# Optimization experiments

Measured on AMD Instinct MI355X. Metric: run time of the kernel, lower is better.

The kernel has to match this reference:

```python
import jax, jax.numpy as jnp
import numpy as np

B, T, C, H = 4, 2048, 1024, 16
D = C // H  # head dim = 64

def setup_inputs() -> dict:
    key = jax.random.key(0)
    k1, k2, k3 = jax.random.split(key, 3)
    s = 1.0 / np.sqrt(C)
    return {
        "x": jax.random.normal(k1, (B, T, C), dtype=jnp.float32),
        "W_attn": jax.random.normal(k2, (C, 3 * C), dtype=jnp.float32) * s,
        "b_attn": jnp.zeros((3 * C,), dtype=jnp.float32),
        "W_proj": jax.random.normal(k3, (C, C), dtype=jnp.float32) * s,
        "b_proj": jnp.zeros((C,), dtype=jnp.float32),
    }

def reference(x, W_attn, b_attn, W_proj, b_proj):
    qkv = x @ W_attn + b_attn                      # [B,T,3C]
    q, k, v = jnp.split(qkv, 3, axis=-1)
    # [B,T,C] -> [B,H,T,D]
    q = q.reshape(B, T, H, D).transpose(0, 2, 1, 3)
    k = k.reshape(B, T, H, D).transpose(0, 2, 1, 3)
    v = v.reshape(B, T, H, D).transpose(0, 2, 1, 3)
    scale = 1.0 / np.sqrt(D)
    att = jnp.einsum('bhqd,bhkd->bhqk', q, k) * scale   # [B,H,T,T]
    causal = jnp.tril(jnp.ones((T, T), dtype=bool))
    att = jnp.where(causal[None, None], att, jnp.float32(-jnp.inf))
    att = jax.nn.softmax(att, axis=-1)
    y = jnp.einsum('bhqk,bhkd->bhqd', att, v)            # [B,H,T,D]
    y = y.transpose(0, 2, 1, 3).reshape(B, T, C)
    return y @ W_proj + b_proj
```

## Files before the change

kernel.cpp:

```cpp
#include <hip/hip_runtime.h>
#include <cstdint>
#include <cstddef>

typedef __bf16 bf16;
typedef __bf16 bf16x8 __attribute__((ext_vector_type(8)));
typedef __bf16 bf16x4 __attribute__((ext_vector_type(4)));
typedef short  s16x4  __attribute__((ext_vector_type(4)));
typedef float  f32x4  __attribute__((ext_vector_type(4)));

#define MFMA16(a, b, c) __builtin_amdgcn_mfma_f32_16x16x32_bf16((a), (b), (c), 0, 0, 0)

#if __has_builtin(__builtin_amdgcn_mfma_f32_16x16x16bf16_1k)
#define HAVE_K16 1
#else
#define HAVE_K16 0
#endif

constexpr int Bsz = 4;
constexpr int T   = 2048;
constexpr int Cd  = 1024;
constexpr int Hn  = 16;
constexpr int Mrows = Bsz * T;
constexpr int QKV_LD = 3 * Cd;

constexpr float QSCALE = 0.125f * 1.4426950408889634f;

__global__ __launch_bounds__(256) void cvt_f32_bf16(const float* __restrict__ in,
                                                    bf16* __restrict__ out, int n) {
    int i = (blockIdx.x * 256 + threadIdx.x) * 8;
    if (i >= n) return;
    float4 a = *(const float4*)(in + i);
    float4 b = *(const float4*)(in + i + 4);
    bf16x8 o;
    o[0] = (bf16)a.x; o[1] = (bf16)a.y; o[2] = (bf16)a.z; o[3] = (bf16)a.w;
    o[4] = (bf16)b.x; o[5] = (bf16)b.y; o[6] = (bf16)b.z; o[7] = (bf16)b.w;
    *(bf16x8*)(out + i) = o;
}

template <int KDIM, int NDIM>
__global__ __launch_bounds__(256) void transpose_cvt(const float* __restrict__ W,
                                                     bf16* __restrict__ Wt) {
    __shared__ float tile[32][33];
    int k0 = blockIdx.y * 32;
    int n0 = blockIdx.x * 32;
    int tx = threadIdx.x;
    int ty = threadIdx.y;
    #pragma unroll
    for (int r = 0; r < 32; r += 8)
        tile[r + ty][tx] = W[(size_t)(k0 + r + ty) * NDIM + n0 + tx];
    __syncthreads();
    #pragma unroll
    for (int r = 0; r < 32; r += 8)
        Wt[(size_t)(n0 + r + ty) * KDIM + k0 + tx] = (bf16)tile[tx][r + ty];
}

template <int N, bool OUT_BF16>
__global__ __launch_bounds__(256) void gemm_bf16(const bf16* __restrict__ A,
                                                 const bf16* __restrict__ Bt,
                                                 const float* __restrict__ bias,
                                                 void* __restrict__ outp,
                                                 float oscale, int oscale_n) {
    constexpr int K = 1024;
    __shared__ __align__(16) bf16 As[128 * 64];
    __shared__ __align__(16) bf16 Bs[128 * 64];

    const int tid  = threadIdx.x;
    const int w    = tid >> 6;
    const int lane = tid & 63;
    const int wm   = w & 1, wn = w >> 1;
    const int quad = lane >> 4, c16 = lane & 15;
    const int m0 = blockIdx.y * 128, n0 = blockIdx.x * 128;

    const int srow = lane >> 3;
    const int scol = ((lane & 7) ^ srow) * 8;
    const int sw   = c16 & 7;

    f32x4 acc[4][4] = {};

    for (int kt = 0; kt < K / 64; ++kt) {
        const int kk = kt * 64;
        #pragma unroll
        for (int i = 0; i < 4; ++i) {
            const int arow = 32 * w + 8 * i;
            __builtin_amdgcn_global_load_lds(
                (const __attribute__((address_space(1))) void*)(A + (size_t)(m0 + arow + srow) * K + kk + scol),
                (__attribute__((address_space(3))) void*)(&As[arow * 64]),
                16, 0, 0);
            __builtin_amdgcn_global_load_lds(
                (const __attribute__((address_space(1))) void*)(Bt + (size_t)(n0 + arow + srow) * K + kk + scol),
                (__attribute__((address_space(3))) void*)(&Bs[arow * 64]),
                16, 0, 0);
        }
        __syncthreads();

        #pragma unroll
        for (int ks = 0; ks < 2; ++ks) {
            const int go = ((ks * 4 + quad) ^ sw) * 8;
            bf16x8 af[4], bfv[4];
            #pragma unroll
            for (int mb = 0; mb < 4; ++mb)
                af[mb] = *(const bf16x8*)&As[(wm * 64 + mb * 16 + c16) * 64 + go];
            #pragma unroll
            for (int nb = 0; nb < 4; ++nb)
                bfv[nb] = *(const bf16x8*)&Bs[(wn * 64 + nb * 16 + c16) * 64 + go];
            #pragma unroll
            for (int mb = 0; mb < 4; ++mb)
                #pragma unroll
                for (int nb = 0; nb < 4; ++nb)
                    acc[mb][nb] = MFMA16(af[mb], bfv[nb], acc[mb][nb]);
        }
        __syncthreads();
    }

    #pragma unroll
    for (int nb = 0; nb < 4; ++nb) {
        const int n = n0 + wn * 64 + nb * 16 + c16;
        const float bv = bias[n];
        const float sc = (n < oscale_n) ? oscale : 1.0f;
        #pragma unroll
        for (int mb = 0; mb < 4; ++mb) {
            const int mbase = m0 + wm * 64 + mb * 16 + quad * 4;
            #pragma unroll
            for (int r = 0; r < 4; ++r) {
                float v = (acc[mb][nb][r] + bv) * sc;
                if (OUT_BF16)
                    ((bf16*)outp)[(size_t)(mbase + r) * N + n] = (bf16)v;
                else
                    ((float*)outp)[(size_t)(mbase + r) * N + n] = v;
            }
        }
    }
}

__global__ __launch_bounds__(256, 2) void attn_fwd(const bf16* __restrict__ qkv,
                                                   bf16* __restrict__ y) {
    __shared__ __align__(16) bf16 Ks2[2][4096];
    __shared__ __align__(16) bf16 Vs[2][64 * 72];
#if !HAVE_K16
    __shared__ __align__(16) bf16 Ps[4][32 * 72];
#endif

    const int x    = blockIdx.x;
    const int h    = blockIdx.y;
    const int bb   = blockIdx.z;
    const int tid  = threadIdx.x;
    const int w    = tid >> 6;
    const int lane = tid & 63;
    const int quad = lane >> 4, c16 = lane & 15;

    const size_t base = (size_t)(bb * T) * QKV_LD;

    const int g = tid >> 5;
    const int p = tid & 31;

    for (int ph = 0; ph < 2; ++ph) {
        const int qt = ph ? x : (15 - x);
        const int q0 = qt * 128;
        const int rowbase = q0 + w * 32;
        const int last = 2 * qt + 1;

        __syncthreads();

        {
            #pragma unroll
            for (int ii = 0; ii < 2; ++ii) {
                const int i = 2 * w + ii;
                const bf16* gp = qkv + base + (size_t)(8 * i + (lane & 7)) * QKV_LD + Cd + h * 64 + (lane >> 3) * 8;
                __builtin_amdgcn_global_load_lds(
                    (const __attribute__((address_space(1))) void*)gp,
                    (__attribute__((address_space(3))) void*)(&Ks2[0][i * 512]), 16, 0, 0);
            }
            const bf16* vp = qkv + base + (size_t)(2 * p) * QKV_LD + 2 * Cd + h * 64 + g * 8;
            bf16x8 va = *(const bf16x8*)vp;
            bf16x8 vb = *(const bf16x8*)(vp + QKV_LD);
            #pragma unroll
            for (int j = 0; j < 8; ++j) {
                union { bf16 hh[2]; uint32_t u; } pk;
                pk.hh[0] = va[j]; pk.hh[1] = vb[j];
                *(uint32_t*)&Vs[0][(8 * g + j) * 72 + 2 * p] = pk.u;
            }
        }

        bf16x8 qf[2][2];
        #pragma unroll
        for (int mb = 0; mb < 2; ++mb) {
            const bf16* qp = qkv + base + (size_t)(rowbase + 16 * mb + c16) * QKV_LD + h * 64 + quad * 8;
            qf[mb][0] = *(const bf16x8*)qp;
            qf[mb][1] = *(const bf16x8*)(qp + 32);
        }

        f32x4 yacc[2][4] = {};
        float lsum[2] = {};

        for (int kt = 0; kt <= last; ++kt) {
            const int cur = kt & 1, nxt = cur ^ 1;
            const int k0 = kt * 64;
            __syncthreads();

            bf16x8 va, vb;
            const bool more = (kt < last);
            if (more) {
                const int kn = k0 + 64;
                #pragma unroll
                for (int ii = 0; ii < 2; ++ii) {
                    const int i = 2 * w + ii;
                    const bf16* gp = qkv + base + (size_t)(kn + 8 * i + (lane & 7)) * QKV_LD + Cd + h * 64 + (lane >> 3) * 8;
                    __builtin_amdgcn_global_load_lds(
                        (const __attribute__((address_space(1))) void*)gp,
                        (__attribute__((address_space(3))) void*)(&Ks2[nxt][i * 512]), 16, 0, 0);
                }
                const bf16* vp = qkv + base + (size_t)(kn + 2 * p) * QKV_LD + 2 * Cd + h * 64 + g * 8;
                va = *(const bf16x8*)vp;
                vb = *(const bf16x8*)(vp + QKV_LD);
            }

            if (k0 <= rowbase + 31) {
                f32x4 s[2][4] = {};
                #pragma unroll
                for (int ks = 0; ks < 2; ++ks)
                    #pragma unroll
                    for (int blk = 0; blk < 4; ++blk) {
                        const bf16x8 kf = *(const bf16x8*)
                            &Ks2[cur][(2 * blk + (c16 >> 3)) * 512 + (4 * ks + quad) * 64 + (c16 & 7) * 8];
                        #pragma unroll
                        for (int mb = 0; mb < 2; ++mb)
                            s[mb][blk] = MFMA16(kf, qf[mb][ks], s[mb][blk]);
                    }

#if HAVE_K16
                union B4 { bf16x4 v; s16x4 s; } pb[2][4];
#endif
                #pragma unroll
                for (int mb = 0; mb < 2; ++mb) {
                    const int rb = rowbase + 16 * mb;
                    const int qglob = rb + c16;
                    const bool needMask = (k0 + 63 > rb);
                    #pragma unroll
                    for (int blk = 0; blk < 4; ++blk) {
                        #pragma unroll
                        for (int r = 0; r < 4; ++r) {
                            const int key = k0 + blk * 16 + quad * 4 + r;
                            float e = s[mb][blk][r];
                            if (needMask) e = (key > qglob) ? -INFINITY : e;
                            float pv = exp2f(e);
                            lsum[mb] += pv;
#if HAVE_K16
                            pb[mb][blk].v[r] = (bf16)pv;
#else
                            Ps[w][(mb * 16 + c16) * 72 + blk * 16 + quad * 4 + r] = (bf16)pv;
#endif
                        }
                    }
                }

#if HAVE_K16
                #pragma unroll
                for (int blk = 0; blk < 4; ++blk)
                    #pragma unroll
                    for (int d16 = 0; d16 < 4; ++d16) {
                        union B4u { bf16x4 v; s16x4 s; } vf;
                        vf.v = *(const bf16x4*)&Vs[cur][(d16 * 16 + c16) * 72 + blk * 16 + quad * 4];
                        #pragma unroll
                        for (int mb = 0; mb < 2; ++mb)
                            yacc[mb][d16] = __builtin_amdgcn_mfma_f32_16x16x16bf16_1k(
                                vf.s, pb[mb][blk].s, yacc[mb][d16], 0, 0, 0);
                    }
#else
                asm volatile("s_waitcnt lgkmcnt(0)" ::: "memory");
                #pragma unroll
                for (int ks = 0; ks < 2; ++ks) {
                    bf16x8 pf0 = *(const bf16x8*)&Ps[w][(0 * 16 + c16) * 72 + ks * 32 + quad * 8];
                    bf16x8 pf1 = *(const bf16x8*)&Ps[w][(1 * 16 + c16) * 72 + ks * 32 + quad * 8];
                    #pragma unroll
                    for (int d16 = 0; d16 < 4; ++d16) {
                        const bf16x8 vfr = *(const bf16x8*)&Vs[cur][(d16 * 16 + c16) * 72 + ks * 32 + quad * 8];
                        yacc[0][d16] = MFMA16(pf0, vfr, yacc[0][d16]);
                        yacc[1][d16] = MFMA16(pf1, vfr, yacc[1][d16]);
                    }
                }
#endif
            }

            if (more) {
                #pragma unroll
                for (int j = 0; j < 8; ++j) {
                    union { bf16 hh[2]; uint32_t u; } pk;
                    pk.hh[0] = va[j]; pk.hh[1] = vb[j];
                    *(uint32_t*)&Vs[nxt][(8 * g + j) * 72 + 2 * p] = pk.u;
                }
            }
        }

        #pragma unroll
        for (int mb = 0; mb < 2; ++mb) {
            lsum[mb] += __shfl_xor(lsum[mb], 16);
            lsum[mb] += __shfl_xor(lsum[mb], 32);
        }

#if HAVE_K16
        #pragma unroll
        for (int mb = 0; mb < 2; ++mb) {
            const float inv = 1.f / lsum[mb];
            const int row = rowbase + 16 * mb + c16;
            bf16* yp = y + (size_t)(bb * T + row) * Cd + h * 64;
            #pragma unroll
            for (int d16 = 0; d16 < 4; ++d16) {
                bf16x4 o;
                #pragma unroll
                for (int r = 0; r < 4; ++r)
                    o[r] = (bf16)(yacc[mb][d16][r] * inv);
                *(bf16x4*)(yp + d16 * 16 + quad * 4) = o;
            }
        }
#else
        #pragma unroll
        for (int mb = 0; mb < 2; ++mb)
            #pragma unroll
            for (int r = 0; r < 4; ++r) {
                const float invq = 1.f / __shfl(lsum[mb], quad * 4 + r);
                const int row = rowbase + 16 * mb + quad * 4 + r;
                bf16* yp = y + (size_t)(bb * T + row) * Cd + h * 64;
                #pragma unroll
                for (int d16 = 0; d16 < 4; ++d16)
                    yp[d16 * 16 + c16] = (bf16)(yacc[mb][d16][r] * invq);
            }
#endif
    }
}

extern "C" void kernel_launch(void* const* d_in, const int* in_sizes, int n_in,
                              void* d_out, int out_size, void* d_ws, size_t ws_size,
                              hipStream_t stream) {
    const float* x      = (const float*)d_in[0];
    const float* W_attn = (const float*)d_in[1];
    const float* b_attn = (const float*)d_in[2];
    const float* W_proj = (const float*)d_in[3];
    const float* b_proj = (const float*)d_in[4];
    float* out = (float*)d_out;

    bf16* xb   = (bf16*)d_ws;
    bf16* Wat  = xb  + (size_t)Mrows * Cd;
    bf16* Wpt  = Wat + (size_t)QKV_LD * Cd;
    bf16* qkv  = Wpt + (size_t)Cd * Cd;
    bf16* yb   = qkv + (size_t)Mrows * QKV_LD;

    cvt_f32_bf16<<<(Mrows * Cd) / (256 * 8), 256, 0, stream>>>(x, xb, Mrows * Cd);
    transpose_cvt<Cd, QKV_LD><<<dim3(QKV_LD / 32, Cd / 32), dim3(32, 8), 0, stream>>>(W_attn, Wat);
    transpose_cvt<Cd, Cd><<<dim3(Cd / 32, Cd / 32), dim3(32, 8), 0, stream>>>(W_proj, Wpt);

    gemm_bf16<QKV_LD, true><<<dim3(QKV_LD / 128, Mrows / 128), 256, 0, stream>>>(
        xb, Wat, b_attn, qkv, QSCALE, Cd);

    attn_fwd<<<dim3(8, Hn, Bsz), 256, 0, stream>>>(qkv, yb);

    gemm_bf16<Cd, false><<<dim3(Cd / 128, Mrows / 128), 256, 0, stream>>>(
        yb, Wpt, b_proj, out, 1.0f, 0);
}
```

Before: 282.4 us.

## Split attention KV range across two blocks and combine partial outputs

```diff
diff --git a/kernel.cpp b/kernel.cpp
--- a/kernel.cpp
+++ b/kernel.cpp
@@ -14,6 +14,12 @@
 #define HAVE_K16 1
 #else
 #define HAVE_K16 0
+#endif
+
+#if __has_builtin(__builtin_amdgcn_exp2f)
+#define EXP2(x) __builtin_amdgcn_exp2f(x)
+#else
+#define EXP2(x) exp2f(x)
 #endif
 
 constexpr int Bsz = 4;
@@ -133,7 +139,9 @@
 }
 
 __global__ __launch_bounds__(256, 2) void attn_fwd(const bf16* __restrict__ qkv,
-                                                   bf16* __restrict__ y) {
+                                                   bf16* __restrict__ yp0,
+                                                   bf16* __restrict__ yp1,
+                                                   float* __restrict__ lp) {
     __shared__ __align__(16) bf16 Ks2[2][4096];
     __shared__ __align__(16) bf16 Vs[2][64 * 72];
 #if !HAVE_K16
@@ -141,6 +149,8 @@
 #endif
 
     const int x    = blockIdx.x;
+    const int xq   = x >> 1;
+    const int sgl  = x & 1;
     const int h    = blockIdx.y;
     const int bb   = blockIdx.z;
     const int tid  = threadIdx.x;
@@ -153,24 +163,29 @@
     const int g = tid >> 5;
     const int p = tid & 31;
 
+    bf16* __restrict__ ydst = sgl ? yp1 : yp0;
+    float* __restrict__ ldst = lp + (size_t)sgl * Mrows * Hn;
+
     for (int ph = 0; ph < 2; ++ph) {
-        const int qt = ph ? x : (15 - x);
+        const int qt = ph ? xq : (15 - xq);
         const int q0 = qt * 128;
         const int rowbase = q0 + w * 32;
-        const int last = 2 * qt + 1;
+        const int start = sgl ? (qt + 1) : 0;
+        const int nkt = qt + 1;
 
         __syncthreads();
 
         {
+            const int kb = start * 64;
             #pragma unroll
             for (int ii = 0; ii < 2; ++ii) {
                 const int i = 2 * w + ii;
-                const bf16* gp = qkv + base + (size_t)(8 * i + (lane & 7)) * QKV_LD + Cd + h * 64 + (lane >> 3) * 8;
+                const bf16* gp = qkv + base + (size_t)(kb + 8 * i + (lane & 7)) * QKV_LD + Cd + h * 64 + (lane >> 3) * 8;
                 __builtin_amdgcn_global_load_lds(
                     (const __attribute__((address_space(1))) void*)gp,
                     (__attribute__((address_space(3))) void*)(&Ks2[0][i * 512]), 16, 0, 0);
             }
-            const bf16* vp = qkv + base + (size_t)(2 * p) * QKV_LD + 2 * Cd + h * 64 + g * 8;
+            const bf16* vp = qkv + base + (size_t)(kb + 2 * p) * QKV_LD + 2 * Cd + h * 64 + g * 8;
             bf16x8 va = *(const bf16x8*)vp;
             bf16x8 vb = *(const bf16x8*)(vp + QKV_LD);
             #pragma unroll
@@ -192,13 +207,13 @@
         f32x4 yacc[2][4] = {};
         float lsum[2] = {};
 
-        for (int kt = 0; kt <= last; ++kt) {
-            const int cur = kt & 1, nxt = cur ^ 1;
-            const int k0 = kt * 64;
+        for (int j = 0; j < nkt; ++j) {
+            const int cur = j & 1, nxt = cur ^ 1;
+            const int k0 = (start + j) * 64;
             __syncthreads();
 
             bf16x8 va, vb;
-            const bool more = (kt < last);
+            const bool more = (j + 1 < nkt);
             if (more) {
                 const int kn = k0 + 64;
                 #pragma unroll
@@ -242,7 +257,7 @@
                             const int key = k0 + blk * 16 + quad * 4 + r;
                             float e = s[mb][blk][r];
                             if (needMask) e = (key > qglob) ? -INFINITY : e;
-                            float pv = exp2f(e);
+                            float pv = EXP2(e);
                             lsum[mb] += pv;
 #if HAVE_K16
                             pb[mb][blk].v[r] = (bf16)pv;
@@ -283,10 +298,10 @@
 
             if (more) {
                 #pragma unroll
-                for (int j = 0; j < 8; ++j) {
+                for (int j2 = 0; j2 < 8; ++j2) {
                     union { bf16 hh[2]; uint32_t u; } pk;
-                    pk.hh[0] = va[j]; pk.hh[1] = vb[j];
-                    *(uint32_t*)&Vs[nxt][(8 * g + j) * 72 + 2 * p] = pk.u;
+                    pk.hh[0] = va[j2]; pk.hh[1] = vb[j2];
+                    *(uint32_t*)&Vs[nxt][(8 * g + j2) * 72 + 2 * p] = pk.u;
                 }
             }
         }
@@ -300,32 +315,53 @@
 #if HAVE_K16
         #pragma unroll
         for (int mb = 0; mb < 2; ++mb) {
-            const float inv = 1.f / lsum[mb];
             const int row = rowbase + 16 * mb + c16;
-            bf16* yp = y + (size_t)(bb * T + row) * Cd + h * 64;
+            bf16* yw = ydst + (size_t)(bb * T + row) * Cd + h * 64;
             #pragma unroll
             for (int d16 = 0; d16 < 4; ++d16) {
                 bf16x4 o;
                 #pragma unroll
                 for (int r = 0; r < 4; ++r)
-                    o[r] = (bf16)(yacc[mb][d16][r] * inv);
-                *(bf16x4*)(yp + d16 * 16 + quad * 4) = o;
-            }
+                    o[r] = (bf16)(yacc[mb][d16][r]);
+                *(bf16x4*)(yw + d16 * 16 + quad * 4) = o;
+            }
+            if (quad == 0)
+                ldst[(size_t)(bb * T + row) * Hn + h] = lsum[mb];
         }
 #else
         #pragma unroll
         for (int mb = 0; mb < 2; ++mb)
             #pragma unroll
             for (int r = 0; r < 4; ++r) {
-                const float invq = 1.f / __shfl(lsum[mb], quad * 4 + r);
+                const float lsv = __shfl(lsum[mb], quad * 4 + r);
                 const int row = rowbase + 16 * mb + quad * 4 + r;
-                bf16* yp = y + (size_t)(bb * T + row) * Cd + h * 64;
+                bf16* yw = ydst + (size_t)(bb * T + row) * Cd + h * 64;
                 #pragma unroll
                 for (int d16 = 0; d16 < 4; ++d16)
-                    yp[d16 * 16 + c16] = (bf16)(yacc[mb][d16][r] * invq);
+                    yw[d16 * 16 + c16] = (bf16)(yacc[mb][d16][r]);
+                if (c16 == 0)
+                    ldst[(size_t)(bb * T + row) * Hn + h] = lsv;
             }
 #endif
     }
+}
+
+__global__ __launch_bounds__(256) void attn_combine(const bf16* __restrict__ yp0,
+                                                    const bf16* __restrict__ yp1,
+                                                    const float* __restrict__ lp,
+                                                    bf16* __restrict__ y) {
+    int i = (blockIdx.x * 256 + threadIdx.x) * 8;
+    int row = i >> 10;
+    int hh  = (i & 1023) >> 6;
+    float l = lp[(size_t)row * Hn + hh] + lp[(size_t)Mrows * Hn + (size_t)row * Hn + hh];
+    float inv = 1.f / l;
+    bf16x8 a = *(const bf16x8*)(yp0 + i);
+    bf16x8 b = *(const bf16x8*)(yp1 + i);
+    bf16x8 o;
+    #pragma unroll
+    for (int j = 0; j < 8; ++j)
+        o[j] = (bf16)(((float)a[j] + (float)b[j]) * inv);
+    *(bf16x8*)(y + i) = o;
 }
 
 extern "C" void kernel_launch(void* const* d_in, const int* in_sizes, int n_in,
@@ -343,6 +379,8 @@
     bf16* Wpt  = Wat + (size_t)QKV_LD * Cd;
     bf16* qkv  = Wpt + (size_t)Cd * Cd;
     bf16* yb   = qkv + (size_t)Mrows * QKV_LD;
+    bf16* yp1  = yb  + (size_t)Mrows * Cd;
+    float* lp  = (float*)(yp1 + (size_t)Mrows * Cd);
 
     cvt_f32_bf16<<<(Mrows * Cd) / (256 * 8), 256, 0, stream>>>(x, xb, Mrows * Cd);
     transpose_cvt<Cd, QKV_LD><<<dim3(QKV_LD / 32, Cd / 32), dim3(32, 8), 0, stream>>>(W_attn, Wat);
@@ -351,7 +389,8 @@
     gemm_bf16<QKV_LD, true><<<dim3(QKV_LD / 128, Mrows / 128), 256, 0, stream>>>(
         xb, Wat, b_attn, qkv, QSCALE, Cd);
 
-    attn_fwd<<<dim3(8, Hn, Bsz), 256, 0, stream>>>(qkv, yb);
+    attn_fwd<<<dim3(16, Hn, Bsz), 256, 0, stream>>>(qkv, yb, yp1, lp);
+    attn_combine<<<(Mrows * Cd) / (256 * 8), 256, 0, stream>>>(yb, yp1, lp, yb);
 
     gemm_bf16<Cd, false><<<dim3(Cd / 128, Mrows / 128), 256, 0, stream>>>(
         yb, Wpt, b_proj, out, 1.0f, 0);
```

Result: no change. 278.1 us (median of 2 runs) (-1.5%).
